# Kernel tuning notes

Hardware: AMD Instinct MI355X
Metric: run time of the kernel (lower is better)

The kernel has to match this reference:

```python
import jax, jax.numpy as jnp
import numpy as np

DMODEL = 1024
NHEAD = 16
HDIM = DMODEL // NHEAD
CTXLEN = 2048
BATCH = 2


def setup_inputs() -> dict:
    key = jax.random.key(0)
    k_x, k_qkv, k_pw, k_pb = jax.random.split(key, 4)
    x = jax.random.normal(k_x, (BATCH, CTXLEN, DMODEL), dtype=jnp.float32)
    # nn.Linear weights: stored as [out, in]; init scale ~ 1/sqrt(in)
    s = 1.0 / np.sqrt(DMODEL)
    w_qkv = jax.random.uniform(k_qkv, (3 * DMODEL, DMODEL), minval=-s, maxval=s, dtype=jnp.float32)
    w_proj = jax.random.uniform(k_pw, (DMODEL, DMODEL), minval=-s, maxval=s, dtype=jnp.float32)
    b_proj = jax.random.uniform(k_pb, (DMODEL,), minval=-s, maxval=s, dtype=jnp.float32)
    return {"x": x, "w_qkv": w_qkv, "w_proj": w_proj, "b_proj": b_proj}


def reference(x, w_qkv, w_proj, b_proj):
    b, t, c = x.shape
    qkv = jnp.einsum('btc,oc->bto', x, w_qkv)  # [b, t, 3c]
    q, k, v = jnp.split(qkv, 3, axis=-1)
    # [b, nhead, t, hdim]
    q = q.reshape(b, t, NHEAD, HDIM).transpose(0, 2, 1, 3)
    k = k.reshape(b, t, NHEAD, HDIM).transpose(0, 2, 1, 3)
    v = v.reshape(b, t, NHEAD, HDIM).transpose(0, 2, 1, 3)
    # NOTE: original code MULTIPLIES by sqrt(hdim) (not the usual divide)
    att = jnp.einsum('bhqd,bhkd->bhqk', q, k) * (HDIM ** 0.5)
    causal = jnp.tril(jnp.ones((t, t), dtype=bool))  # [t, t]
    att = jnp.where(causal[None, None], att, -jnp.inf)
    att = jax.nn.softmax(att, axis=-1)
    y = jnp.einsum('bhqk,bhkd->bhqd', att, v)
    y = y.transpose(0, 2, 1, 3).reshape(b, t, c)
    return jnp.einsum('btc,oc->bto', y, w_proj) + b_proj
```

## Files before the change

### kernel.cpp

```cpp
#include <hip/hip_runtime.h>
#include <hip/hip_bf16.h>

#define DMODEL 1024
#define NHEAD 16
#define HDIM 64
#define CTXLEN 2048
#define BATCH 2
#define M_TOTAL (BATCH * CTXLEN)

typedef unsigned short ushort_t;
typedef __attribute__((ext_vector_type(8))) _Float16 f16x8;
typedef __attribute__((ext_vector_type(8))) unsigned short u16x8;
typedef __attribute__((ext_vector_type(4))) float f32x4;
typedef __attribute__((ext_vector_type(4))) unsigned short u16x4;

#define SCALE_LOG2 11.5415603271f

__device__ __forceinline__ unsigned short f32_f16(float f) {
    return __builtin_bit_cast(unsigned short, (_Float16)f);
}
__device__ __forceinline__ float f16_f32(unsigned short h) {
    return (float)__builtin_bit_cast(_Float16, h);
}
__device__ __forceinline__ float fast_exp2(float x) {
    return __builtin_amdgcn_exp2f(x);
}
__device__ __forceinline__ f32x4 mfma16f(f16x8 a, f16x8 b, f32x4 c) {
    return __builtin_amdgcn_mfma_f32_16x16x32_f16(a, b, c, 0, 0, 0);
}
__device__ __forceinline__ void gload_lds16(const ushort_t* g, ushort_t* l) {
    __builtin_amdgcn_global_load_lds(
        (const __attribute__((address_space(1))) void*)g,
        (__attribute__((address_space(3))) void*)l, 16, 0, 0);
}
__device__ __forceinline__ int unit_off(int qt) {
    if (qt < 8)  return qt;
    if (qt < 16) return 8 + (qt - 8) * 2;
    if (qt < 24) return 24 + (qt - 16) * 3;
    return 48 + (qt - 24) * 4;
}

__global__ __launch_bounds__(256)
void conv3_f32_f16(const float* __restrict__ a, ushort_t* __restrict__ da, int na4,
                   const float* __restrict__ b, ushort_t* __restrict__ db, int nb4,
                   const float* __restrict__ c, ushort_t* __restrict__ dc, int nc4) {
    const int n = na4 + nb4 + nc4;
    for (int i = blockIdx.x * blockDim.x + threadIdx.x; i < n;
         i += gridDim.x * blockDim.x) {
        const float* s; ushort_t* d; int j = i;
        if (j < na4) { s = a; d = da; }
        else if (j - na4 < nb4) { j -= na4; s = b; d = db; }
        else { j -= na4 + nb4; s = c; d = dc; }
        const float4 v = reinterpret_cast<const float4*>(s)[j];
        u16x4 o;
        o[0] = f32_f16(v.x); o[1] = f32_f16(v.y);
        o[2] = f32_f16(v.z); o[3] = f32_f16(v.w);
        reinterpret_cast<u16x4*>(d)[j] = o;
    }
}

template<int BN, bool QKV_EPI>
__global__ __launch_bounds__(256)
void gemm_f16_nt(const ushort_t* __restrict__ A, const ushort_t* __restrict__ B,
                 const float* __restrict__ bias, float* __restrict__ C,
                 ushort_t* __restrict__ qf, ushort_t* __restrict__ kf,
                 ushort_t* __restrict__ vt,
                 int M, int N, int K) {
    constexpr int NF = BN / 32;
    constexpr int BOFF = 8192;
    constexpr int BCHUNK = BN * 8;
    constexpr int LDSZ = QKV_EPI ? 17408 : (BOFF + BN * 64);
    __shared__ ushort_t lds[LDSZ];

    int bx, by;
    {
        const int gx  = gridDim.x;
        const int nwg = gx * (int)gridDim.y;
        const int cpx = nwg >> 3;
        int flat = (int)blockIdx.y * gx + (int)blockIdx.x;
        flat = (flat & 7) * cpx + (flat >> 3);
        bx = flat % gx;
        by = flat / gx;
    }

    const int tid  = threadIdx.x;
    const int lane = tid & 63;
    const int wave = tid >> 6;
    const int lc   = lane & 15;
    const int lg   = lane >> 4;
    const int wr   = wave >> 1;
    const int wc   = wave & 1;
    const int row0 = by * 128;
    const int col0 = bx * BN;

    int aoff[4][2], boff[NF][2];
    #pragma unroll
    for (int m = 0; m < 4; ++m) {
        const int ra = wr * 64 + m * 16 + lc;
        #pragma unroll
        for (int kk = 0; kk < 2; ++kk)
            aoff[m][kk] = ra * 64 + (((kk * 4 + lg) ^ (ra & 7)) * 8);
    }
    #pragma unroll
    for (int n = 0; n < NF; ++n) {
        const int rb = wc * (NF * 16) + n * 16 + lc;
        #pragma unroll
        for (int kk = 0; kk < 2; ++kk)
            boff[n][kk] = rb * 64 + (((kk * 4 + lg) ^ (rb & 7)) * 8);
    }

    f32x4 acc[4][NF];
    const f32x4 zero4 = {0.f, 0.f, 0.f, 0.f};
    #pragma unroll
    for (int m = 0; m < 4; ++m)
        #pragma unroll
        for (int n = 0; n < NF; ++n) acc[m][n] = zero4;

    const int NT = K >> 6;

    auto stage = [&](int kt) {
        const int ko = kt * 64;
        #pragma unroll
        for (int i = 0; i < 4; ++i) {
            const int c  = tid + i * 256;
            const int r  = c >> 3;
            const int sg = (c & 7) ^ (r & 7);
            gload_lds16(A + (size_t)(row0 + r) * K + ko + sg * 8, &lds[c * 8]);
        }
        #pragma unroll
        for (int i = 0; i < BCHUNK / 256; ++i) {
            const int c  = tid + i * 256;
            const int r  = c >> 3;
            const int sg = (c & 7) ^ (r & 7);
            gload_lds16(B + (size_t)(col0 + r) * K + ko + sg * 8, &lds[BOFF + c * 8]);
        }
    };

    stage(0);
    for (int kt = 0; kt < NT; ++kt) {
        __syncthreads();
        f16x8 fa[2][4], fb[2][NF];
        #pragma unroll
        for (int kk = 0; kk < 2; ++kk) {
            #pragma unroll
            for (int m = 0; m < 4; ++m)
                fa[kk][m] = *reinterpret_cast<const f16x8*>(&lds[aoff[m][kk]]);
            #pragma unroll
            for (int n = 0; n < NF; ++n)
                fb[kk][n] = *reinterpret_cast<const f16x8*>(&lds[BOFF + boff[n][kk]]);
        }
        __syncthreads();
        if (kt + 1 < NT) stage(kt + 1);
        #pragma unroll
        for (int kk = 0; kk < 2; ++kk)
            #pragma unroll
            for (int m = 0; m < 4; ++m)
                #pragma unroll
                for (int n = 0; n < NF; ++n)
                    acc[m][n] = mfma16f(fa[kk][m], fb[kk][n], acc[m][n]);
    }

    if (!QKV_EPI) {
        #pragma unroll
        for (int m = 0; m < 4; ++m)
            #pragma unroll
            for (int i = 0; i < 4; ++i) {
                const int r = row0 + wr * 64 + m * 16 + lg * 4 + i;
                #pragma unroll
                for (int n = 0; n < NF; ++n) {
                    const int c = col0 + wc * (NF * 16) + n * 16 + lc;
                    C[(size_t)r * N + c] = acc[m][n][i] + bias[c];
                }
            }
    } else {
        const int sec_blk = col0 >> 10;
        if (sec_blk == 2) {
            __syncthreads();
            #pragma unroll
            for (int m = 0; m < 4; ++m)
                #pragma unroll
                for (int n = 0; n < NF; ++n) {
                    const int lcol = wc * (NF * 16) + n * 16 + lc;
                    const int lrow = wr * 64 + m * 16 + lg * 4;
                    u16x4 o;
                    #pragma unroll
                    for (int i = 0; i < 4; ++i) o[i] = f32_f16(acc[m][n][i]);
                    *reinterpret_cast<u16x4*>(&lds[lcol * 136 + lrow]) = o;
                }
            __syncthreads();
            const int bb   = row0 >> 11;
            const int t0   = row0 & 2047;
            const int lcol = tid >> 1;
            const int th   = (tid & 1) * 64;
            const int ch   = (col0 - 2048) + lcol;
            ushort_t* dst = vt + ((size_t)(bb * NHEAD + (ch >> 6)) * HDIM + (ch & 63)) * CTXLEN
                            + t0 + th;
            #pragma unroll
            for (int j = 0; j < 8; ++j)
                *reinterpret_cast<u16x8*>(&dst[j * 8]) =
                    *reinterpret_cast<const u16x8*>(&lds[lcol * 136 + th + j * 8]);
        } else {
            #pragma unroll
            for (int m = 0; m < 4; ++m)
                #pragma unroll
                for (int i = 0; i < 4; ++i) {
                    const int r = row0 + wr * 64 + m * 16 + lg * 4 + i;
                    const int bb = r >> 11;
                    const int t  = r & 2047;
                    #pragma unroll
                    for (int n = 0; n < NF; ++n) {
                        const int cg = col0 + wc * (NF * 16) + n * 16 + lc;
                        const int ch = cg & 1023;
                        const int hh = ch >> 6;
                        const int d  = ch & 63;
                        const size_t off = (((size_t)(bb * NHEAD + hh)) * CTXLEN + t) * HDIM + d;
                        float v = acc[m][n][i];
                        if (sec_blk == 0) {
                            qf[off] = f32_f16(v * SCALE_LOG2);
                        } else {
                            kf[off] = f32_f16(v);
                        }
                    }
                }
        }
    }
}

__global__ __launch_bounds__(256)
void attn_fwd7(const ushort_t* __restrict__ qf, const ushort_t* __restrict__ kf,
               const ushort_t* __restrict__ vt,
               ushort_t* __restrict__ py, float* __restrict__ pml,
               ushort_t* __restrict__ yb) {
    __shared__ ushort_t KH[2][4096];
    __shared__ ushort_t VT[2][4096];
    __shared__ ushort_t Ps[4][16][64];

    const int id    = blockIdx.x;
    const int bh    = id & 31;
    const int u_off = 79 - (id >> 5);
    int qt, u;
    if (u_off < 8)       { qt = u_off;                          u = 0; }
    else if (u_off < 24) { const int t = u_off - 8;  qt = 8  + (t >> 1); u = t & 1; }
    else if (u_off < 48) { const int t = u_off - 24; const int q3 = t / 3; qt = 16 + q3; u = t - q3 * 3; }
    else                 { const int t = u_off - 48; qt = 24 + (t >> 2); u = t & 3; }
    const int total = qt + 1;
    const int nu    = (qt >> 3) + 1;
    const int base  = total / nu, rem = total % nu;
    const int kb0   = u * base + (u < rem ? u : rem);
    const int len   = base + (u < rem ? 1 : 0);
    const int slot  = bh * 80 + u_off;

    const int tid  = threadIdx.x;
    const int wave = tid >> 6;
    const int lane = tid & 63;
    const int lc   = lane & 15;
    const int lg   = lane >> 4;

    const ushort_t* kfb = kf + (size_t)bh * CTXLEN * HDIM;
    const ushort_t* vtb = vt + (size_t)bh * HDIM * CTXLEN;

    const int cA = tid, cB = 256 + tid;
    const int rA = cA >> 3, sgA = (cA & 7) ^ (rA & 7);
    const int rB = cB >> 3, sgB = (cB & 7) ^ (rB & 7);

    auto stage = [&](int kb, int buf) {
        const size_t koff = (size_t)(kb * 64);
        gload_lds16(kfb + (koff + rA) * HDIM + sgA * 8, &KH[buf][cA * 8]);
        gload_lds16(kfb + (koff + rB) * HDIM + sgB * 8, &KH[buf][cB * 8]);
        gload_lds16(vtb + (size_t)rA * CTXLEN + kb * 64 + sgA * 8, &VT[buf][cA * 8]);
        gload_lds16(vtb + (size_t)rB * CTXLEN + kb * 64 + sgB * 8, &VT[buf][cB * 8]);
    };

    const size_t qrow = (size_t)bh * CTXLEN + qt * 64 + wave * 16 + lc;
    f16x8 qfr[2];
    #pragma unroll
    for (int ds = 0; ds < 2; ++ds)
        qfr[ds] = *reinterpret_cast<const f16x8*>(&qf[qrow * HDIM + ds * 32 + lg * 8]);

    const f32x4 zero4 = {0.f, 0.f, 0.f, 0.f};
    f32x4 yacc[4];
    #pragma unroll
    for (int t = 0; t < 4; ++t) yacc[t] = zero4;
    float m_i = -1e30f, l_i = 0.f;

    stage(kb0, 0);
    __syncthreads();

    int cur = 0;
    for (int s = 0; s < len; ++s) {
        const int kb = kb0 + s;
        if (s + 1 < len) stage(kb + 1, cur ^ 1);

        f16x8 kfr[4][2];
        #pragma unroll
        for (int tc = 0; tc < 4; ++tc) {
            const int rk = tc * 16 + lc;
            #pragma unroll
            for (int ds = 0; ds < 2; ++ds) {
                const int a = rk * 64 + (((ds * 4 + lg) ^ (rk & 7)) * 8);
                kfr[tc][ds] = *reinterpret_cast<const f16x8*>(&KH[cur][a]);
            }
        }
        f16x8 vf[4][2];
        #pragma unroll
        for (int t = 0; t < 4; ++t) {
            const int rv = t * 16 + lc;
            #pragma unroll
            for (int ks = 0; ks < 2; ++ks) {
                const int a = rv * 64 + (((ks * 4 + lg) ^ (rv & 7)) * 8);
                vf[t][ks] = *reinterpret_cast<const f16x8*>(&VT[cur][a]);
            }
        }

        f32x4 sacc[4];
        #pragma unroll
        for (int tc = 0; tc < 4; ++tc) sacc[tc] = zero4;
        __builtin_amdgcn_s_setprio(1);
        #pragma unroll
        for (int tc = 0; tc < 4; ++tc)
            #pragma unroll
            for (int ds = 0; ds < 2; ++ds)
                sacc[tc] = mfma16f(kfr[tc][ds], qfr[ds], sacc[tc]);
        __builtin_amdgcn_s_setprio(0);

        float p[4][4];
        #pragma unroll
        for (int tc = 0; tc < 4; ++tc)
            #pragma unroll
            for (int i = 0; i < 4; ++i)
                p[tc][i] = sacc[tc][i];
        if (kb == qt) {
            const int q_loc = wave * 16 + lc;
            #pragma unroll
            for (int tc = 0; tc < 4; ++tc)
                #pragma unroll
                for (int i = 0; i < 4; ++i)
                    if ((tc * 16 + lg * 4 + i) > q_loc) p[tc][i] = -1e30f;
        }
        float mx = p[0][0];
        #pragma unroll
        for (int tc = 0; tc < 4; ++tc)
            #pragma unroll
            for (int i = 0; i < 4; ++i) mx = fmaxf(mx, p[tc][i]);
        mx = fmaxf(mx, __shfl_xor(mx, 16));
        mx = fmaxf(mx, __shfl_xor(mx, 32));

        if (__all(mx <= m_i + 8.0f)) {
            float psum = 0.f;
            #pragma unroll
            for (int tc = 0; tc < 4; ++tc)
                #pragma unroll
                for (int i = 0; i < 4; ++i) {
                    const float e = fast_exp2(p[tc][i] - m_i);
                    p[tc][i] = e;
                    psum += e;
                }
            psum += __shfl_xor(psum, 16);
            psum += __shfl_xor(psum, 32);
            l_i += psum;
        } else {
            const float mnew = fmaxf(m_i, mx);
            const float corr = fast_exp2(m_i - mnew);
            float psum = 0.f;
            #pragma unroll
            for (int tc = 0; tc < 4; ++tc)
                #pragma unroll
                for (int i = 0; i < 4; ++i) {
                    const float e = fast_exp2(p[tc][i] - mnew);
                    p[tc][i] = e;
                    psum += e;
                }
            psum += __shfl_xor(psum, 16);
            psum += __shfl_xor(psum, 32);
            l_i = l_i * corr + psum;
            m_i = mnew;
            #pragma unroll
            for (int t = 0; t < 4; ++t) yacc[t] *= corr;
        }

        #pragma unroll
        for (int tc = 0; tc < 4; ++tc) {
            const int eb = tc * 16 + lg * 4;
            const int se = ((((eb >> 3) ^ (lc & 7)) << 3) | (eb & 7));
            u16x4 pk;
            #pragma unroll
            for (int i = 0; i < 4; ++i) pk[i] = f32_f16(p[tc][i]);
            *reinterpret_cast<u16x4*>(&Ps[wave][lc][se]) = pk;
        }
        f16x8 pa[2];
        #pragma unroll
        for (int ks = 0; ks < 2; ++ks) {
            const int sl = ((ks * 4 + lg) ^ (lc & 7)) << 3;
            pa[ks] = *reinterpret_cast<const f16x8*>(&Ps[wave][lc][sl]);
        }
        __builtin_amdgcn_s_setprio(1);
        #pragma unroll
        for (int t = 0; t < 4; ++t)
            #pragma unroll
            for (int ks = 0; ks < 2; ++ks)
                yacc[t] = mfma16f(vf[t][ks], pa[ks], yacc[t]);
        __builtin_amdgcn_s_setprio(0);

        __syncthreads();
        cur ^= 1;
    }

    const int row = wave * 16 + lc;
    if (nu == 1) {
        const float inv = 1.0f / l_i;
        const int b = bh >> 4, h = bh & 15;
        ushort_t* dst = yb + (size_t)(b * CTXLEN + qt * 64 + row) * DMODEL + h * HDIM;
        #pragma unroll
        for (int t = 0; t < 4; ++t) {
            u16x4 o;
            #pragma unroll
            for (int i = 0; i < 4; ++i) o[i] = f32_f16(yacc[t][i] * inv);
            *reinterpret_cast<u16x4*>(&dst[t * 16 + lg * 4]) = o;
        }
    } else {
        ushort_t* prow = py + ((size_t)slot * 64 + row) * 64;
        #pragma unroll
        for (int t = 0; t < 4; ++t) {
            u16x4 o;
            #pragma unroll
            for (int i = 0; i < 4; ++i) o[i] = f32_f16(yacc[t][i]);
            *reinterpret_cast<u16x4*>(&prow[t * 16 + lg * 4]) = o;
        }
        if (lg == 0) {
            pml[(size_t)slot * 128 + row]      = m_i;
            pml[(size_t)slot * 128 + 64 + row] = l_i;
        }
    }
}

__global__ __launch_bounds__(256)
void merge_attn(const ushort_t* __restrict__ py, const float* __restrict__ pml,
                ushort_t* __restrict__ yb) {
    const int qt  = 8 + blockIdx.x;
    const int bh  = blockIdx.y;
    const int b   = bh >> 4;
    const int h   = bh & 15;
    const int tid = threadIdx.x;
    const int row = tid >> 2;
    const int d0  = (tid & 3) * 16;

    const int nu    = (qt >> 3) + 1;
    const int sbase = bh * 80 + unit_off(qt);

    float mu[4], lu[4];
    float M = -1e30f;
    #pragma unroll
    for (int u = 0; u < 4; ++u) {
        if (u < nu) {
            mu[u] = pml[(size_t)(sbase + u) * 128 + row];
            lu[u] = pml[(size_t)(sbase + u) * 128 + 64 + row];
            M = fmaxf(M, mu[u]);
        } else { mu[u] = -1e30f; lu[u] = 0.f; }
    }
    float w[4], ltot = 0.f;
    #pragma unroll
    for (int u = 0; u < 4; ++u) {
        w[u] = (u < nu) ? fast_exp2(mu[u] - M) : 0.f;
        ltot += w[u] * lu[u];
    }

    float y[16];
    #pragma unroll
    for (int j = 0; j < 16; ++j) y[j] = 0.f;
    #pragma unroll
    for (int u = 0; u < 4; ++u) {
        if (u < nu) {
            const ushort_t* pr = py + ((size_t)(sbase + u) * 64 + row) * 64 + d0;
            const u16x8 a = *reinterpret_cast<const u16x8*>(&pr[0]);
            const u16x8 c = *reinterpret_cast<const u16x8*>(&pr[8]);
            #pragma unroll
            for (int j = 0; j < 8; ++j) {
                y[j]     += w[u] * f16_f32(a[j]);
                y[8 + j] += w[u] * f16_f32(c[j]);
            }
        }
    }
    const float inv = 1.0f / ltot;
    ushort_t* dst = yb + (size_t)(b * CTXLEN + qt * 64 + row) * DMODEL + h * HDIM + d0;
    u16x8 o0, o1;
    #pragma unroll
    for (int j = 0; j < 8; ++j) {
        o0[j] = f32_f16(y[j] * inv);
        o1[j] = f32_f16(y[8 + j] * inv);
    }
    *reinterpret_cast<u16x8*>(&dst[0]) = o0;
    *reinterpret_cast<u16x8*>(&dst[8]) = o1;
}

extern "C" void kernel_launch(void* const* d_in, const int* in_sizes, int n_in,
                              void* d_out, int out_size, void* d_ws, size_t ws_size,
                              hipStream_t stream) {
    const float* x      = (const float*)d_in[0];
    const float* w_qkv  = (const float*)d_in[1];
    const float* w_proj = (const float*)d_in[2];
    const float* b_proj = (const float*)d_in[3];
    float* out = (float*)d_out;

    char* ws = (char*)d_ws;
    ushort_t* wqf = (ushort_t*)(ws);
    ushort_t* wpf = (ushort_t*)(ws + 6291456);
    ushort_t* xf  = (ushort_t*)(ws + 8388608);
    ushort_t* qf  = (ushort_t*)(ws + 16777216);
    ushort_t* kf  = (ushort_t*)(ws + 25165824);
    ushort_t* vt  = (ushort_t*)(ws + 41943040);
    ushort_t* py  = (ushort_t*)(ws + 50331648);
    float*    pml = (float*)   (ws + 71303168);
    ushort_t* yb  = xf;

    const dim3 blk(256);

    conv3_f32_f16<<<dim3(2048), blk, 0, stream>>>(
        x, xf, M_TOTAL * DMODEL / 4,
        w_qkv, wqf, 3 * DMODEL * DMODEL / 4,
        w_proj, wpf, DMODEL * DMODEL / 4);

    gemm_f16_nt<128, true><<<dim3(3 * DMODEL / 128, M_TOTAL / 128), blk, 0, stream>>>(
        xf, wqf, nullptr, nullptr, qf, kf, vt, M_TOTAL, 3 * DMODEL, DMODEL);

    attn_fwd7<<<dim3(2560), blk, 0, stream>>>(qf, kf, vt, py, pml, yb);
    merge_attn<<<dim3(24, 32), blk, 0, stream>>>(py, pml, yb);

    gemm_f16_nt<64, false><<<dim3(DMODEL / 64, M_TOTAL / 128), blk, 0, stream>>>(
        yb, wpf, b_proj, out, nullptr, nullptr, nullptr, M_TOTAL, DMODEL, DMODEL);
}
```

Measured before the change: 105.3 us.

## Split attention into single-wave blocks with 32-key tiles and per-wave causal skipping

Replaces the 4-wave attention block with one-wave blocks, one per 16-row query slice, each streaming 32-key K/V tiles through its own double-buffered LDS. Without cross-wave sharing, __syncthreads is dropped and each wave can skip the final causal half-tile it never needs. The aim is finer-grained scheduling, less barrier stalling and less masked causal work. In exchange, every wave now loads K/V itself, so global and L2 traffic rise about fourfold and four times as many blocks launch.

```diff
diff --git a/kernel.cpp b/kernel.cpp
--- a/kernel.cpp
+++ b/kernel.cpp
@@ -226,52 +226,54 @@
     }
 }
 
-__global__ __launch_bounds__(256)
-void attn_fwd7(const ushort_t* __restrict__ qf, const ushort_t* __restrict__ kf,
-               const ushort_t* __restrict__ vt,
-               ushort_t* __restrict__ py, float* __restrict__ pml,
-               ushort_t* __restrict__ yb) {
-    __shared__ ushort_t KH[2][4096];
-    __shared__ ushort_t VT[2][4096];
-    __shared__ ushort_t Ps[4][16][64];
+__global__ __launch_bounds__(64)
+void attn_fwd11(const ushort_t* __restrict__ qf, const ushort_t* __restrict__ kf,
+                const ushort_t* __restrict__ vt,
+                ushort_t* __restrict__ py, float* __restrict__ pml,
+                ushort_t* __restrict__ yb) {
+    __shared__ ushort_t KH[2][2048];
+    __shared__ ushort_t VT[2][2048];
+    __shared__ ushort_t Ps[16][32];
 
     const int id    = blockIdx.x;
-    const int bh    = id & 31;
-    const int u_off = 79 - (id >> 5);
+    const int wavq  = id & 3;
+    const int bh    = (id >> 2) & 31;
+    const int u_off = 79 - (id >> 7);
     int qt, u;
     if (u_off < 8)       { qt = u_off;                          u = 0; }
     else if (u_off < 24) { const int t = u_off - 8;  qt = 8  + (t >> 1); u = t & 1; }
     else if (u_off < 48) { const int t = u_off - 24; const int q3 = t / 3; qt = 16 + q3; u = t - q3 * 3; }
     else                 { const int t = u_off - 48; qt = 24 + (t >> 2); u = t & 3; }
-    const int total = qt + 1;
+    const int total32 = 2 * qt + 2;
     const int nu    = (qt >> 3) + 1;
-    const int base  = total / nu, rem = total % nu;
+    const int base  = total32 / nu, rem = total32 % nu;
     const int kb0   = u * base + (u < rem ? u : rem);
-    const int len   = base + (u < rem ? 1 : 0);
+    int       len   = base + (u < rem ? 1 : 0);
+    if (kb0 + len == 2 * qt + 2 && wavq < 2) len -= 1;
     const int slot  = bh * 80 + u_off;
 
-    const int tid  = threadIdx.x;
-    const int wave = tid >> 6;
-    const int lane = tid & 63;
+    const int lane = threadIdx.x;
     const int lc   = lane & 15;
     const int lg   = lane >> 4;
 
     const ushort_t* kfb = kf + (size_t)bh * CTXLEN * HDIM;
     const ushort_t* vtb = vt + (size_t)bh * HDIM * CTXLEN;
 
-    const int cA = tid, cB = 256 + tid;
-    const int rA = cA >> 3, sgA = (cA & 7) ^ (rA & 7);
-    const int rB = cB >> 3, sgB = (cB & 7) ^ (rB & 7);
-
-    auto stage = [&](int kb, int buf) {
-        const size_t koff = (size_t)(kb * 64);
-        gload_lds16(kfb + (koff + rA) * HDIM + sgA * 8, &KH[buf][cA * 8]);
-        gload_lds16(kfb + (koff + rB) * HDIM + sgB * 8, &KH[buf][cB * 8]);
-        gload_lds16(vtb + (size_t)rA * CTXLEN + kb * 64 + sgA * 8, &VT[buf][cA * 8]);
-        gload_lds16(vtb + (size_t)rB * CTXLEN + kb * 64 + sgB * 8, &VT[buf][cB * 8]);
+    auto stage = [&](int kb32, int buf) {
+        const int koff = kb32 * 32;
+        #pragma unroll
+        for (int i = 0; i < 4; ++i) {
+            const int c  = lane + i * 64;
+            const int rk = c >> 3;
+            const int sk = (c & 7) ^ (rk & 7);
+            gload_lds16(kfb + (size_t)(koff + rk) * HDIM + sk * 8, &KH[buf][c * 8]);
+            const int rv = c >> 2;
+            const int sv = (c & 3) ^ (rv & 3);
+            gload_lds16(vtb + (size_t)rv * CTXLEN + koff + sv * 8, &VT[buf][c * 8]);
+        }
     };
 
-    const size_t qrow = (size_t)bh * CTXLEN + qt * 64 + wave * 16 + lc;
+    const size_t qrow = (size_t)bh * CTXLEN + qt * 64 + wavq * 16 + lc;
     f16x8 qfr[2];
     #pragma unroll
     for (int ds = 0; ds < 2; ++ds)
@@ -284,16 +286,16 @@
     float m_i = -1e30f, l_i = 0.f;
 
     stage(kb0, 0);
-    __syncthreads();
-
-    int cur = 0;
+
     for (int s = 0; s < len; ++s) {
-        const int kb = kb0 + s;
-        if (s + 1 < len) stage(kb + 1, cur ^ 1);
-
-        f16x8 kfr[4][2];
-        #pragma unroll
-        for (int tc = 0; tc < 4; ++tc) {
+        const int kb32 = kb0 + s;
+        const int cur  = s & 1;
+
+        asm volatile("s_waitcnt vmcnt(0)" ::: "memory");
+
+        f16x8 kfr[2][2];
+        #pragma unroll
+        for (int tc = 0; tc < 2; ++tc) {
             const int rk = tc * 16 + lc;
             #pragma unroll
             for (int ds = 0; ds < 2; ++ds) {
@@ -301,45 +303,45 @@
                 kfr[tc][ds] = *reinterpret_cast<const f16x8*>(&KH[cur][a]);
             }
         }
-        f16x8 vf[4][2];
+        f16x8 vf[4];
         #pragma unroll
         for (int t = 0; t < 4; ++t) {
             const int rv = t * 16 + lc;
-            #pragma unroll
-            for (int ks = 0; ks < 2; ++ks) {
-                const int a = rv * 64 + (((ks * 4 + lg) ^ (rv & 7)) * 8);
-                vf[t][ks] = *reinterpret_cast<const f16x8*>(&VT[cur][a]);
-            }
-        }
-
-        f32x4 sacc[4];
-        #pragma unroll
-        for (int tc = 0; tc < 4; ++tc) sacc[tc] = zero4;
+            vf[t] = *reinterpret_cast<const f16x8*>(&VT[cur][rv * 32 + ((lg ^ (rv & 3)) * 8)]);
+        }
+
+        if (s + 1 < len) stage(kb32 + 1, cur ^ 1);
+
+        f32x4 sacc[2];
+        #pragma unroll
+        for (int tc = 0; tc < 2; ++tc) sacc[tc] = zero4;
         __builtin_amdgcn_s_setprio(1);
         #pragma unroll
-        for (int tc = 0; tc < 4; ++tc)
+        for (int tc = 0; tc < 2; ++tc)
             #pragma unroll
             for (int ds = 0; ds < 2; ++ds)
                 sacc[tc] = mfma16f(kfr[tc][ds], qfr[ds], sacc[tc]);
         __builtin_amdgcn_s_setprio(0);
 
-        float p[4][4];
-        #pragma unroll
-        for (int tc = 0; tc < 4; ++tc)
+        float p[2][4];
+        #pragma unroll
+        for (int tc = 0; tc < 2; ++tc)
             #pragma unroll
             for (int i = 0; i < 4; ++i)
                 p[tc][i] = sacc[tc][i];
-        if (kb == qt) {
-            const int q_loc = wave * 16 + lc;
-            #pragma unroll
-            for (int tc = 0; tc < 4; ++tc)
-                #pragma unroll
-                for (int i = 0; i < 4; ++i)
-                    if ((tc * 16 + lg * 4 + i) > q_loc) p[tc][i] = -1e30f;
+        if (kb32 >= 2 * qt) {
+            const int q_loc = wavq * 16 + lc;
+            #pragma unroll
+            for (int tc = 0; tc < 2; ++tc)
+                #pragma unroll
+                for (int i = 0; i < 4; ++i) {
+                    const int k_loc = (kb32 & 1) * 32 + tc * 16 + lg * 4 + i;
+                    if (k_loc > q_loc) p[tc][i] = -1e30f;
+                }
         }
         float mx = p[0][0];
         #pragma unroll
-        for (int tc = 0; tc < 4; ++tc)
+        for (int tc = 0; tc < 2; ++tc)
             #pragma unroll
             for (int i = 0; i < 4; ++i) mx = fmaxf(mx, p[tc][i]);
         mx = fmaxf(mx, __shfl_xor(mx, 16));
@@ -348,7 +350,7 @@
         if (__all(mx <= m_i + 8.0f)) {
             float psum = 0.f;
             #pragma unroll
-            for (int tc = 0; tc < 4; ++tc)
+            for (int tc = 0; tc < 2; ++tc)
                 #pragma unroll
                 for (int i = 0; i < 4; ++i) {
                     const float e = fast_exp2(p[tc][i] - m_i);
@@ -363,7 +365,7 @@
             const float corr = fast_exp2(m_i - mnew);
             float psum = 0.f;
             #pragma unroll
-            for (int tc = 0; tc < 4; ++tc)
+            for (int tc = 0; tc < 2; ++tc)
                 #pragma unroll
                 for (int i = 0; i < 4; ++i) {
                     const float e = fast_exp2(p[tc][i] - mnew);
@@ -379,33 +381,24 @@
         }
 
         #pragma unroll
-        for (int tc = 0; tc < 4; ++tc) {
+        for (int tc = 0; tc < 2; ++tc) {
             const int eb = tc * 16 + lg * 4;
-            const int se = ((((eb >> 3) ^ (lc & 7)) << 3) | (eb & 7));
+            const int se = ((((eb >> 3) ^ (lc & 3)) << 3) | (eb & 7));
             u16x4 pk;
             #pragma unroll
             for (int i = 0; i < 4; ++i) pk[i] = f32_f16(p[tc][i]);
-            *reinterpret_cast<u16x4*>(&Ps[wave][lc][se]) = pk;
-        }
-        f16x8 pa[2];
-        #pragma unroll
-        for (int ks = 0; ks < 2; ++ks) {
-            const int sl = ((ks * 4 + lg) ^ (lc & 7)) << 3;
-            pa[ks] = *reinterpret_cast<const f16x8*>(&Ps[wave][lc][sl]);
-        }
+            *reinterpret_cast<u16x4*>(&Ps[lc][se]) = pk;
+        }
+        const f16x8 pa = *reinterpret_cast<const f16x8*>(&Ps[lc][(lg ^ (lc & 3)) * 8]);
+
         __builtin_amdgcn_s_setprio(1);
         #pragma unroll
         for (int t = 0; t < 4; ++t)
-            #pragma unroll
-            for (int ks = 0; ks < 2; ++ks)
-                yacc[t] = mfma16f(vf[t][ks], pa[ks], yacc[t]);
+            yacc[t] = mfma16f(vf[t], pa, yacc[t]);
         __builtin_amdgcn_s_setprio(0);
-
-        __syncthreads();
-        cur ^= 1;
-    }
-
-    const int row = wave * 16 + lc;
+    }
+
+    const int row = wavq * 16 + lc;
     if (nu == 1) {
         const float inv = 1.0f / l_i;
         const int b = bh >> 4, h = bh & 15;
@@ -522,7 +515,7 @@
     gemm_f16_nt<128, true><<<dim3(3 * DMODEL / 128, M_TOTAL / 128), blk, 0, stream>>>(
         xf, wqf, nullptr, nullptr, qf, kf, vt, M_TOTAL, 3 * DMODEL, DMODEL);
 
-    attn_fwd7<<<dim3(2560), blk, 0, stream>>>(qf, kf, vt, py, pml, yb);
+    attn_fwd11<<<dim3(10240), dim3(64), 0, stream>>>(qf, kf, vt, py, pml, yb);
     merge_attn<<<dim3(24, 32), blk, 0, stream>>>(py, pml, yb);
 
     gemm_f16_nt<64, false><<<dim3(DMODEL / 64, M_TOTAL / 128), blk, 0, stream>>>(
```

Result: slower. 155.5 us (+47.6%).
